# Kernel tuning notes

Hardware: AMD Instinct MI355X
Metric: run time of the kernel (lower is better)

Reference implementation:

```python
import jax, jax.numpy as jnp
import numpy as np

N_NODES = 100000
N_EDGES = 1600000
D_IN = 128
D_OUT = 128


def setup_inputs() -> dict:
    key = jax.random.key(0)
    k1, k2, k3 = jax.random.split(key, 3)
    x = jax.random.normal(k1, (N_NODES, D_IN), dtype=jnp.float32)
    edge_indices = jax.random.randint(k2, (2, N_EDGES), 0, N_NODES, dtype=jnp.int64)
    # nn.Linear(input_dim, output_dim, bias=False): weight shape [out, in]
    W = jax.random.normal(k3, (D_OUT, D_IN), dtype=jnp.float32) * (1.0 / np.sqrt(D_IN))
    return {"x": x, "edge_indices": edge_indices, "W": W}


def reference(x, edge_indices, W):
    N = x.shape[0]
    # add self loops (i, i) for every node, as in create_norm_adj_mat
    self_loops = jnp.arange(N, dtype=edge_indices.dtype)
    row = jnp.concatenate([edge_indices[0], self_loops])  # [E+N]
    col = jnp.concatenate([edge_indices[1], self_loops])  # [E+N]
    # degree from row indices (torch.bincount(edge_indices[0]))
    deg = jax.ops.segment_sum(jnp.ones_like(row, dtype=x.dtype), row, num_segments=N)
    deg_rsqrt = jax.lax.rsqrt(deg)  # every node has a self loop -> deg >= 1
    vals = deg_rsqrt[row] * deg_rsqrt[col]  # [E+N] edge weights
    # dense linear projection first (linear(x)), then sparse aggregation
    h = x @ W.T  # [N, D_OUT]
    # (norm_adj_mat @ h)[i] = sum over edges with row==i of vals * h[col]
    agg = jax.ops.segment_sum(vals[:, None] * h[col], row, num_segments=N)  # [N, D_OUT]
    return jax.nn.relu(agg)
```

## Files before the change

### kernel.cpp

```cpp
#include <hip/hip_runtime.h>
#include <hip/hip_bf16.h>

#define D 128
#define SH 8
#define BROWS 256
#define NBK_MAX 512
#define CH 8192

typedef __bf16   bf16x8 __attribute__((ext_vector_type(8)));
typedef float    f32x4  __attribute__((ext_vector_type(4)));
typedef _Float16 f16x2  __attribute__((ext_vector_type(2)));
typedef _Float16 f16x4  __attribute__((ext_vector_type(4)));

__global__ __launch_bounds__(256) void k_zero(int* __restrict__ p, int n) {
    for (int i = blockIdx.x * blockDim.x + threadIdx.x; i < n; i += gridDim.x * blockDim.x)
        p[i] = 0;
}

__global__ __launch_bounds__(256) void k_bucket_count(const int* __restrict__ rows,
                                                      int* __restrict__ bcnt, int E, int NBK) {
    __shared__ int h[NBK_MAX];
    for (int i = threadIdx.x; i < NBK; i += 256) h[i] = 0;
    __syncthreads();
    for (int e = blockIdx.x * blockDim.x + threadIdx.x; e < E; e += gridDim.x * blockDim.x)
        atomicAdd(&h[rows[e] >> SH], 1);
    __syncthreads();
    for (int i = threadIdx.x; i < NBK; i += 256) {
        int v = h[i];
        if (v) atomicAdd(&bcnt[i], v);
    }
}

__global__ __launch_bounds__(512) void k_scan_buckets(const int* __restrict__ bcnt,
                                                      int* __restrict__ boff,
                                                      int* __restrict__ bcur, int NBK, int E) {
    __shared__ int sd[512];
    int t = threadIdx.x;
    int own = (t < NBK) ? bcnt[t] : 0;
    sd[t] = own;
    __syncthreads();
    for (int off = 1; off < 512; off <<= 1) {
        int add = (t >= off) ? sd[t - off] : 0;
        __syncthreads();
        sd[t] += add;
        __syncthreads();
    }
    if (t < NBK) {
        int ex = sd[t] - own;
        boff[t] = ex;
        bcur[t] = ex;
    }
    if (t == 0) boff[NBK] = E;
}

__global__ __launch_bounds__(256) void k_pairs(const int* __restrict__ rows,
                                               const int* __restrict__ cols,
                                               int* __restrict__ bcur,
                                               unsigned* __restrict__ pairs, int E, int NBK) {
    __shared__ int h[NBK_MAX];
    int e0 = blockIdx.x * CH;
    if (e0 >= E) return;
    int e1 = min(E, e0 + CH);
    for (int i = threadIdx.x; i < NBK; i += 256) h[i] = 0;
    __syncthreads();
    for (int e = e0 + threadIdx.x; e < e1; e += 256)
        atomicAdd(&h[rows[e] >> SH], 1);
    __syncthreads();
    for (int b = threadIdx.x; b < NBK; b += 256) {
        int v = h[b];
        h[b] = v ? atomicAdd(&bcur[b], v) : 0;
    }
    __syncthreads();
    for (int e = e0 + threadIdx.x; e < e1; e += 256) {
        int r = rows[e];
        int b = r >> SH;
        int p = atomicAdd(&h[b], 1);
        pairs[p] = ((unsigned)(r & (BROWS - 1)) << 24) | (unsigned)cols[e];
    }
}

__global__ __launch_bounds__(256) void k_bucket_hist(const unsigned* __restrict__ pairs,
                                                     const int* __restrict__ boff,
                                                     int* __restrict__ cnt, int N) {
    __shared__ int h[BROWS];
    int b = blockIdx.x;
    int lim = min(N - (b << SH), BROWS);
    h[threadIdx.x] = 0;
    __syncthreads();
    int p0 = boff[b], p1 = boff[b + 1];
    for (int p = p0 + threadIdx.x; p < p1; p += 256)
        atomicAdd(&h[pairs[p] >> 24], 1);
    __syncthreads();
    if (threadIdx.x < lim) cnt[(b << SH) + threadIdx.x] = h[threadIdx.x];
}

__global__ __launch_bounds__(256) void k_chunk_sum(const int* __restrict__ cnt,
                                                   int* __restrict__ bsum, int N) {
    __shared__ int sd[256];
    int base = blockIdx.x * 1024;
    int t = threadIdx.x;
    int s = 0;
#pragma unroll
    for (int k = 0; k < 4; ++k) {
        int i = base + t * 4 + k;
        if (i < N) s += cnt[i];
    }
    sd[t] = s;
    __syncthreads();
    for (int off = 128; off > 0; off >>= 1) {
        if (t < off) sd[t] += sd[t + off];
        __syncthreads();
    }
    if (t == 0) bsum[blockIdx.x] = sd[0];
}

__global__ __launch_bounds__(1024) void k_scan_tops(const int* __restrict__ bsum,
                                                    int* __restrict__ boff2, int nb,
                                                    int* __restrict__ row_start, int N, int E) {
    __shared__ int sd[1024];
    int t = threadIdx.x;
    int own = (t < nb) ? bsum[t] : 0;
    sd[t] = own;
    __syncthreads();
    for (int off = 1; off < 1024; off <<= 1) {
        int add = (t >= off) ? sd[t - off] : 0;
        __syncthreads();
        sd[t] += add;
        __syncthreads();
    }
    if (t < nb) boff2[t] = sd[t] - own;
    if (t == 0) row_start[N] = E;
}

__global__ __launch_bounds__(256) void k_scan_chunk(const int* __restrict__ cnt,
                                                    const int* __restrict__ boff2,
                                                    int* __restrict__ row_start,
                                                    float* __restrict__ dr, int N) {
    __shared__ int tsum[256];
    int base = blockIdx.x * 1024;
    int t = threadIdx.x;
    int v[4];
    int s = 0;
#pragma unroll
    for (int k = 0; k < 4; ++k) {
        int i = base + t * 4 + k;
        v[k] = (i < N) ? cnt[i] : 0;
        s += v[k];
    }
    tsum[t] = s;
    __syncthreads();
    for (int off = 1; off < 256; off <<= 1) {
        int add = (t >= off) ? tsum[t - off] : 0;
        __syncthreads();
        tsum[t] += add;
        __syncthreads();
    }
    int run = boff2[blockIdx.x] + tsum[t] - s;
#pragma unroll
    for (int k = 0; k < 4; ++k) {
        int i = base + t * 4 + k;
        if (i < N) {
            row_start[i] = run;
            dr[i] = rsqrtf((float)(v[k] + 1));
            run += v[k];
        }
    }
}

__global__ __launch_bounds__(256) void k_place(const unsigned* __restrict__ pairs,
                                               const int* __restrict__ boff,
                                               const int* __restrict__ row_start,
                                               int* __restrict__ csr_col, int N) {
    __shared__ int cur[BROWS];
    int b = blockIdx.x;
    int lim = min(N - (b << SH), BROWS);
    if (threadIdx.x < lim) cur[threadIdx.x] = row_start[(b << SH) + threadIdx.x];
    __syncthreads();
    int p0 = boff[b], p1 = boff[b + 1];
    for (int p = p0 + threadIdx.x; p < p1; p += 256) {
        unsigned v = pairs[p];
        int rl = v >> 24;
        int c  = v & 0xFFFFFF;
        int q = atomicAdd(&cur[rl], 1);
        csr_col[q] = c;
    }
}

__global__ __launch_bounds__(256) void k_half(const float4* __restrict__ x4,
                                              f16x4* __restrict__ xh4, int n4) {
    for (int i = blockIdx.x * blockDim.x + threadIdx.x; i < n4; i += gridDim.x * blockDim.x) {
        float4 v = x4[i];
        xh4[i] = (f16x4){(_Float16)v.x, (_Float16)v.y, (_Float16)v.z, (_Float16)v.w};
    }
}

__global__ __launch_bounds__(256) void k_gather_h(const int* __restrict__ row_start,
                                                  const int* __restrict__ csr_col,
                                                  const _Float16* __restrict__ xh,
                                                  const float* __restrict__ dr,
                                                  float* __restrict__ out, int N) {
    int lane = threadIdx.x & 63;
    int gw = (blockIdx.x * blockDim.x + threadIdx.x) >> 6;
    int nw = (gridDim.x * blockDim.x) >> 6;
    for (int r = gw; r < N; r += nw) {
        float drr = dr[r];
        int beg = row_start[r], end = row_start[r + 1];
        const f16x2 xs = *(const f16x2*)&xh[(size_t)r * D + lane * 2];
        float s = drr * drr;
        float a0 = s * (float)xs[0], a1 = s * (float)xs[1];
        for (int cb = beg; cb < end; cb += 64) {
            int m = end - cb;
            if (m > 64) m = 64;
            int   cidx = (lane < m) ? csr_col[cb + lane] : 0;
            float cdr  = (lane < m) ? dr[cidx] : 0.f;
            int j = 0;
            for (; j + 8 <= m; j += 8) {
#pragma unroll
                for (int u = 0; u < 8; u += 4) {
                    int c0 = __shfl(cidx, j + u);
                    int c1 = __shfl(cidx, j + u + 1);
                    int c2 = __shfl(cidx, j + u + 2);
                    int c3 = __shfl(cidx, j + u + 3);
                    float v0 = drr * __shfl(cdr, j + u);
                    float v1 = drr * __shfl(cdr, j + u + 1);
                    float v2 = drr * __shfl(cdr, j + u + 2);
                    float v3 = drr * __shfl(cdr, j + u + 3);
                    const f16x2 p0 = *(const f16x2*)&xh[(size_t)c0 * D + lane * 2];
                    const f16x2 p1 = *(const f16x2*)&xh[(size_t)c1 * D + lane * 2];
                    const f16x2 p2 = *(const f16x2*)&xh[(size_t)c2 * D + lane * 2];
                    const f16x2 p3 = *(const f16x2*)&xh[(size_t)c3 * D + lane * 2];
                    a0 = fmaf(v0, (float)p0[0], a0); a1 = fmaf(v0, (float)p0[1], a1);
                    a0 = fmaf(v1, (float)p1[0], a0); a1 = fmaf(v1, (float)p1[1], a1);
                    a0 = fmaf(v2, (float)p2[0], a0); a1 = fmaf(v2, (float)p2[1], a1);
                    a0 = fmaf(v3, (float)p3[0], a0); a1 = fmaf(v3, (float)p3[1], a1);
                }
            }
            for (; j < m; ++j) {
                int   c = __shfl(cidx, j);
                float v = drr * __shfl(cdr, j);
                const f16x2 p = *(const f16x2*)&xh[(size_t)c * D + lane * 2];
                a0 = fmaf(v, (float)p[0], a0);
                a1 = fmaf(v, (float)p[1], a1);
            }
        }
        float2 o;
        o.x = a0;
        o.y = a1;
        *(float2*)&out[(size_t)r * D + lane * 2] = o;
    }
}

__global__ __launch_bounds__(256) void k_gather(const int* __restrict__ row_start,
                                                const int* __restrict__ csr_col,
                                                const float* __restrict__ x,
                                                const float* __restrict__ dr,
                                                float* __restrict__ out, int N) {
    int lane = threadIdx.x & 63;
    int gw = (blockIdx.x * blockDim.x + threadIdx.x) >> 6;
    int nw = (gridDim.x * blockDim.x) >> 6;
    for (int r = gw; r < N; r += nw) {
        float drr = dr[r];
        int beg = row_start[r], end = row_start[r + 1];
        const float2 xs = *(const float2*)&x[(size_t)r * D + lane * 2];
        float s = drr * drr;
        float a0 = s * xs.x, a1 = s * xs.y;
        for (int cb = beg; cb < end; cb += 64) {
            int m = end - cb;
            if (m > 64) m = 64;
            int   cidx = (lane < m) ? csr_col[cb + lane] : 0;
            float cdr  = (lane < m) ? dr[cidx] : 0.f;
            int j = 0;
            for (; j + 4 <= m; j += 4) {
                int c0 = __shfl(cidx, j);
                int c1 = __shfl(cidx, j + 1);
                int c2 = __shfl(cidx, j + 2);
                int c3 = __shfl(cidx, j + 3);
                float v0 = drr * __shfl(cdr, j);
                float v1 = drr * __shfl(cdr, j + 1);
                float v2 = drr * __shfl(cdr, j + 2);
                float v3 = drr * __shfl(cdr, j + 3);
                const float2 p0 = *(const float2*)&x[(size_t)c0 * D + lane * 2];
                const float2 p1 = *(const float2*)&x[(size_t)c1 * D + lane * 2];
                const float2 p2 = *(const float2*)&x[(size_t)c2 * D + lane * 2];
                const float2 p3 = *(const float2*)&x[(size_t)c3 * D + lane * 2];
                a0 = fmaf(v0, p0.x, a0); a1 = fmaf(v0, p0.y, a1);
                a0 = fmaf(v1, p1.x, a0); a1 = fmaf(v1, p1.y, a1);
                a0 = fmaf(v2, p2.x, a0); a1 = fmaf(v2, p2.y, a1);
                a0 = fmaf(v3, p3.x, a0); a1 = fmaf(v3, p3.y, a1);
            }
            for (; j < m; ++j) {
                int   c = __shfl(cidx, j);
                float v = drr * __shfl(cdr, j);
                const float2 p = *(const float2*)&x[(size_t)c * D + lane * 2];
                a0 = fmaf(v, p.x, a0);
                a1 = fmaf(v, p.y, a1);
            }
        }
        float2 o;
        o.x = a0;
        o.y = a1;
        *(float2*)&out[(size_t)r * D + lane * 2] = o;
    }
}

#define CT 8
#define KS 4

__global__ __launch_bounds__(256) void k_project_mfma(const float* __restrict__ W,
                                                      float* __restrict__ out, int N) {
    __shared__ bf16x8 Bhi[CT * KS * 64];
    __shared__ bf16x8 Blo[CT * KS * 64];

    for (int f = threadIdx.x; f < CT * KS * 64; f += 256) {
        int l  = f & 63;
        int ks = (f >> 6) & 3;
        int ct = f >> 8;
        int o  = ct * 16 + (l & 15);
        int k0 = ks * 32 + ((l >> 4) * 8);
        const float* src = &W[o * D + k0];
        bf16x8 hi, lo;
#pragma unroll
        for (int i = 0; i < 8; ++i) {
            float v  = src[i];
            __bf16 h = (__bf16)v;
            float  r = v - (float)h;
            hi[i] = h;
            lo[i] = (__bf16)r;
        }
        Bhi[f] = hi;
        Blo[f] = lo;
    }
    __syncthreads();

    int lane = threadIdx.x & 63;
    int wib  = threadIdx.x >> 6;
    int gw   = blockIdx.x * 4 + wib;
    int nw   = gridDim.x * 4;
    int nt   = N >> 4;

    int arow  = lane & 15;
    int kbase = (lane >> 4) * 8;

    for (int t = gw; t < nt; t += nw) {
        int row = t * 16 + arow;
        const float* arp = &out[(size_t)row * D + kbase];

        bf16x8 Ahi[KS], Alo[KS];
#pragma unroll
        for (int ks = 0; ks < KS; ++ks) {
            float4 v0 = *(const float4*)&arp[ks * 32];
            float4 v1 = *(const float4*)&arp[ks * 32 + 4];
            float va[8] = {v0.x, v0.y, v0.z, v0.w, v1.x, v1.y, v1.z, v1.w};
            bf16x8 hi, lo;
#pragma unroll
            for (int i = 0; i < 8; ++i) {
                float v  = va[i];
                __bf16 h = (__bf16)v;
                float  r = v - (float)h;
                hi[i] = h;
                lo[i] = (__bf16)r;
            }
            Ahi[ks] = hi;
            Alo[ks] = lo;
        }

        f32x4 acc[CT];
#pragma unroll
        for (int ct = 0; ct < CT; ++ct) acc[ct] = (f32x4){0.f, 0.f, 0.f, 0.f};

#pragma unroll
        for (int ks = 0; ks < KS; ++ks) {
#pragma unroll
            for (int ct = 0; ct < CT; ++ct) {
                bf16x8 bh = Bhi[(ct * KS + ks) * 64 + lane];
                bf16x8 bl = Blo[(ct * KS + ks) * 64 + lane];
                acc[ct] = __builtin_amdgcn_mfma_f32_16x16x32_bf16(Ahi[ks], bh, acc[ct], 0, 0, 0);
                acc[ct] = __builtin_amdgcn_mfma_f32_16x16x32_bf16(Alo[ks], bh, acc[ct], 0, 0, 0);
                acc[ct] = __builtin_amdgcn_mfma_f32_16x16x32_bf16(Ahi[ks], bl, acc[ct], 0, 0, 0);
            }
        }

        int orow = t * 16 + (lane >> 4) * 4;
        int ocol = lane & 15;
#pragma unroll
        for (int ct = 0; ct < CT; ++ct) {
#pragma unroll
            for (int reg = 0; reg < 4; ++reg) {
                out[(size_t)(orow + reg) * D + ct * 16 + ocol] = fmaxf(acc[ct][reg], 0.f);
            }
        }
    }
}

__global__ __launch_bounds__(256) void k_init_deg(int* __restrict__ deg, int n) {
    for (int i = blockIdx.x * blockDim.x + threadIdx.x; i < n; i += gridDim.x * blockDim.x)
        deg[i] = 1;
}
__global__ __launch_bounds__(256) void k_count_atomic(const int* __restrict__ rows,
                                                      int* __restrict__ cnt, int E) {
    for (int e = blockIdx.x * blockDim.x + threadIdx.x; e < E; e += gridDim.x * blockDim.x)
        atomicAdd(&cnt[rows[e]], 1);
}
__global__ __launch_bounds__(256) void k_rsqrt(float* __restrict__ buf, int n) {
    const int* di = (const int*)buf;
    for (int i = blockIdx.x * blockDim.x + threadIdx.x; i < n; i += gridDim.x * blockDim.x) {
        int v = di[i];
        buf[i] = rsqrtf((float)v);
    }
}
__global__ __launch_bounds__(256) void k_init_out(const float4* __restrict__ x4,
                                                  const float* __restrict__ dr,
                                                  float4* __restrict__ out4, int n4) {
    for (int i = blockIdx.x * blockDim.x + threadIdx.x; i < n4; i += gridDim.x * blockDim.x) {
        float d = dr[i >> 5];
        float s = d * d;
        float4 v = x4[i];
        out4[i] = make_float4(v.x * s, v.y * s, v.z * s, v.w * s);
    }
}
__global__ __launch_bounds__(256) void k_edges(const int* __restrict__ rows,
                                               const int* __restrict__ cols,
                                               const float* __restrict__ x,
                                               const float* __restrict__ dr,
                                               float* __restrict__ out, int E) {
    int lane = threadIdx.x & 63;
    int wib  = threadIdx.x >> 6;
    int gw   = blockIdx.x * 4 + wib;
    int nw   = gridDim.x * 4;
    for (int e = gw; e < E; e += nw) {
        int r = rows[e];
        int c = cols[e];
        float val = dr[r] * dr[c];
        const float2 xv = *(const float2*)&x[(size_t)c * D + lane * 2];
        float* po = &out[(size_t)r * D + lane * 2];
        unsafeAtomicAdd(po,     val * xv.x);
        unsafeAtomicAdd(po + 1, val * xv.y);
    }
}

extern "C" void kernel_launch(void* const* d_in, const int* in_sizes, int n_in,
                              void* d_out, int out_size, void* d_ws, size_t ws_size,
                              hipStream_t stream) {
    const float* x   = (const float*)d_in[0];
    const int*   idx = (const int*)d_in[1];
    const float* W   = (const float*)d_in[2];
    float*       out = (float*)d_out;

    int N = in_sizes[0] / D;
    int E = in_sizes[1] / 2;
    const int* rows = idx;
    const int* cols = idx + E;

    int NBK = (N + BROWS - 1) >> SH;
    int nb  = (N + 1023) / 1024;

    size_t off = 0;
    size_t o_pairs = off;  off += (size_t)E;
    size_t o_csr   = off;  off += (size_t)E;
    size_t o_cnt   = off;  off += (size_t)N;
    size_t o_rs    = off;  off += (size_t)N + 1;
    size_t o_dr    = off;  off += (size_t)N;
    size_t o_bsum  = off;  off += (size_t)nb;
    size_t o_boff2 = off;  off += (size_t)nb;
    size_t o_bcnt  = off;  off += (size_t)NBK;
    size_t o_boff  = off;  off += (size_t)NBK + 1;
    size_t o_bcur  = off;  off += (size_t)NBK;
    off = (off + 3) & ~(size_t)3;
    size_t o_xh    = off;  off += ((size_t)N * D) / 2;
    size_t need_full = off * 4;
    size_t need_base = o_xh * 4;

    int* wsw = (int*)d_ws;

    bool shape_ok = (NBK <= NBK_MAX) && (nb <= 1024) && ((N & 15) == 0) && (N < (1 << 24));

    if (shape_ok && ws_size >= need_base) {
        unsigned* pairs     = (unsigned*)(wsw + o_pairs);
        int*      csr_col   = wsw + o_csr;
        int*      cnt       = wsw + o_cnt;
        int*      row_start = wsw + o_rs;
        float*    dr        = (float*)(wsw + o_dr);
        int*      bsum      = wsw + o_bsum;
        int*      boff2     = wsw + o_boff2;
        int*      bcnt      = wsw + o_bcnt;
        int*      boff      = wsw + o_boff;
        int*      bcur      = wsw + o_bcur;
        _Float16* xh        = (_Float16*)(wsw + o_xh);

        k_zero<<<(NBK + 255) / 256, 256, 0, stream>>>(bcnt, NBK);
        k_bucket_count<<<512, 256, 0, stream>>>(rows, bcnt, E, NBK);
        k_scan_buckets<<<1, 512, 0, stream>>>(bcnt, boff, bcur, NBK, E);
        k_pairs<<<(E + CH - 1) / CH, 256, 0, stream>>>(rows, cols, bcur, pairs, E, NBK);
        k_bucket_hist<<<NBK, 256, 0, stream>>>(pairs, boff, cnt, N);
        k_chunk_sum<<<nb, 256, 0, stream>>>(cnt, bsum, N);
        k_scan_tops<<<1, 1024, 0, stream>>>(bsum, boff2, nb, row_start, N, E);
        k_scan_chunk<<<nb, 256, 0, stream>>>(cnt, boff2, row_start, dr, N);
        k_place<<<NBK, 256, 0, stream>>>(pairs, boff, row_start, csr_col, N);

        if (ws_size >= need_full) {
            k_half<<<2048, 256, 0, stream>>>((const float4*)x, (f16x4*)xh, N * (D / 4));
            k_gather_h<<<4096, 256, 0, stream>>>(row_start, csr_col, xh, dr, out, N);
        } else {
            k_gather<<<4096, 256, 0, stream>>>(row_start, csr_col, x, dr, out, N);
        }
        int nt = N >> 4;
        k_project_mfma<<<(nt + 3) / 4, 256, 0, stream>>>(W, out, N);
    } else {
        int*   deg = (int*)d_ws;
        float* dr  = (float*)d_ws;
        k_init_deg<<<(N + 255) / 256, 256, 0, stream>>>(deg, N);
        k_count_atomic<<<2048, 256, 0, stream>>>(rows, deg, E);
        k_rsqrt<<<(N + 255) / 256, 256, 0, stream>>>(dr, N);
        int n4 = N * (D / 4);
        k_init_out<<<4096, 256, 0, stream>>>((const float4*)x, dr, (float4*)out, n4);
        k_edges<<<4096, 256, 0, stream>>>(rows, cols, x, dr, out, E);
        int nt = N >> 4;
        k_project_mfma<<<(nt + 3) / 4, 256, 0, stream>>>(W, out, N);
    }
}
```

Before: 230.3 us.

## Fuse gather aggregation with MFMA projection and prescale fp16 features by degree

```diff
diff --git a/kernel.cpp b/kernel.cpp
--- a/kernel.cpp
+++ b/kernel.cpp
@@ -6,11 +6,13 @@
 #define BROWS 256
 #define NBK_MAX 512
 #define CH 8192
+#define CT 8
+#define KS 4
 
 typedef __bf16   bf16x8 __attribute__((ext_vector_type(8)));
 typedef float    f32x4  __attribute__((ext_vector_type(4)));
-typedef _Float16 f16x2  __attribute__((ext_vector_type(2)));
 typedef _Float16 f16x4  __attribute__((ext_vector_type(4)));
+typedef _Float16 f16x8  __attribute__((ext_vector_type(8)));
 
 __global__ __launch_bounds__(256) void k_zero(int* __restrict__ p, int n) {
     for (int i = blockIdx.x * blockDim.x + threadIdx.x; i < n; i += gridDim.x * blockDim.x)
@@ -186,67 +188,166 @@
     }
 }
 
-__global__ __launch_bounds__(256) void k_half(const float4* __restrict__ x4,
-                                              f16x4* __restrict__ xh4, int n4) {
+__global__ __launch_bounds__(256) void k_half_s(const float4* __restrict__ x4,
+                                                const float* __restrict__ dr,
+                                                f16x4* __restrict__ xh4, int n4) {
     for (int i = blockIdx.x * blockDim.x + threadIdx.x; i < n4; i += gridDim.x * blockDim.x) {
+        float d = dr[i >> 5];
         float4 v = x4[i];
-        xh4[i] = (f16x4){(_Float16)v.x, (_Float16)v.y, (_Float16)v.z, (_Float16)v.w};
-    }
-}
-
-__global__ __launch_bounds__(256) void k_gather_h(const int* __restrict__ row_start,
-                                                  const int* __restrict__ csr_col,
-                                                  const _Float16* __restrict__ xh,
-                                                  const float* __restrict__ dr,
-                                                  float* __restrict__ out, int N) {
+        xh4[i] = (f16x4){(_Float16)(v.x * d), (_Float16)(v.y * d),
+                         (_Float16)(v.z * d), (_Float16)(v.w * d)};
+    }
+}
+
+__global__ __launch_bounds__(256) void k_prepW(const float* __restrict__ W,
+                                               bf16x8* __restrict__ Whi,
+                                               bf16x8* __restrict__ Wlo) {
+    for (int f = blockIdx.x * blockDim.x + threadIdx.x; f < CT * KS * 64;
+         f += gridDim.x * blockDim.x) {
+        int l  = f & 63;
+        int ks = (f >> 6) & 3;
+        int ct = f >> 8;
+        int o  = ct * 16 + (l & 15);
+        int k0 = ks * 32 + ((l >> 4) * 8);
+        const float* src = &W[o * D + k0];
+        bf16x8 hi, lo;
+#pragma unroll
+        for (int i = 0; i < 8; ++i) {
+            float v  = src[i];
+            __bf16 h = (__bf16)v;
+            hi[i] = h;
+            lo[i] = (__bf16)(v - (float)h);
+        }
+        Whi[f] = hi;
+        Wlo[f] = lo;
+    }
+}
+
+__global__ __launch_bounds__(256) void k_gp(const int* __restrict__ row_start,
+                                            const int* __restrict__ csr_col,
+                                            const _Float16* __restrict__ xh,
+                                            const float* __restrict__ dr,
+                                            const bf16x8* __restrict__ Whi,
+                                            const bf16x8* __restrict__ Wlo,
+                                            float* __restrict__ out, int NT) {
+    __shared__ float lds[4][16][132];
     int lane = threadIdx.x & 63;
+    int wib  = threadIdx.x >> 6;
+    float (*patch)[132] = lds[wib];
+
     int gw = (blockIdx.x * blockDim.x + threadIdx.x) >> 6;
     int nw = (gridDim.x * blockDim.x) >> 6;
-    for (int r = gw; r < N; r += nw) {
-        float drr = dr[r];
-        int beg = row_start[r], end = row_start[r + 1];
-        const f16x2 xs = *(const f16x2*)&xh[(size_t)r * D + lane * 2];
-        float s = drr * drr;
-        float a0 = s * (float)xs[0], a1 = s * (float)xs[1];
-        for (int cb = beg; cb < end; cb += 64) {
-            int m = end - cb;
-            if (m > 64) m = 64;
-            int   cidx = (lane < m) ? csr_col[cb + lane] : 0;
-            float cdr  = (lane < m) ? dr[cidx] : 0.f;
-            int j = 0;
-            for (; j + 8 <= m; j += 8) {
-#pragma unroll
-                for (int u = 0; u < 8; u += 4) {
-                    int c0 = __shfl(cidx, j + u);
-                    int c1 = __shfl(cidx, j + u + 1);
-                    int c2 = __shfl(cidx, j + u + 2);
-                    int c3 = __shfl(cidx, j + u + 3);
-                    float v0 = drr * __shfl(cdr, j + u);
-                    float v1 = drr * __shfl(cdr, j + u + 1);
-                    float v2 = drr * __shfl(cdr, j + u + 2);
-                    float v3 = drr * __shfl(cdr, j + u + 3);
-                    const f16x2 p0 = *(const f16x2*)&xh[(size_t)c0 * D + lane * 2];
-                    const f16x2 p1 = *(const f16x2*)&xh[(size_t)c1 * D + lane * 2];
-                    const f16x2 p2 = *(const f16x2*)&xh[(size_t)c2 * D + lane * 2];
-                    const f16x2 p3 = *(const f16x2*)&xh[(size_t)c3 * D + lane * 2];
-                    a0 = fmaf(v0, (float)p0[0], a0); a1 = fmaf(v0, (float)p0[1], a1);
-                    a0 = fmaf(v1, (float)p1[0], a0); a1 = fmaf(v1, (float)p1[1], a1);
-                    a0 = fmaf(v2, (float)p2[0], a0); a1 = fmaf(v2, (float)p2[1], a1);
-                    a0 = fmaf(v3, (float)p3[0], a0); a1 = fmaf(v3, (float)p3[1], a1);
+
+    int eslot = lane >> 4;
+    int dbase = (lane & 15) * 8;
+
+    for (int t = gw; t < NT; t += nw) {
+        int r0 = t * 16;
+        int   rs16 = (lane < 17) ? row_start[r0 + lane] : 0;
+        float dr16 = (lane < 16) ? dr[r0 + lane] : 0.f;
+
+        for (int rr = 0; rr < 16; ++rr) {
+            int r   = r0 + rr;
+            int beg = __shfl(rs16, rr);
+            int end = __shfl(rs16, rr + 1);
+            float drr = __shfl(dr16, rr);
+
+            float acc[8];
+            {
+                f16x8 xs = *(const f16x8*)&xh[(size_t)r * D + dbase];
+                float w = (eslot == 0) ? 1.0f : 0.0f;
+#pragma unroll
+                for (int i = 0; i < 8; ++i) acc[i] = w * (float)xs[i];
+            }
+
+            for (int cb = beg; cb < end; cb += 64) {
+                int m = end - cb;
+                if (m > 64) m = 64;
+                int cidx = (lane < m) ? csr_col[cb + lane] : 0;
+                int g = 0;
+                for (; g + 16 <= m; g += 16) {
+                    int c0 = __shfl(cidx, g + eslot);
+                    int c1 = __shfl(cidx, g + 4 + eslot);
+                    int c2 = __shfl(cidx, g + 8 + eslot);
+                    int c3 = __shfl(cidx, g + 12 + eslot);
+                    f16x8 p0 = *(const f16x8*)&xh[(size_t)c0 * D + dbase];
+                    f16x8 p1 = *(const f16x8*)&xh[(size_t)c1 * D + dbase];
+                    f16x8 p2 = *(const f16x8*)&xh[(size_t)c2 * D + dbase];
+                    f16x8 p3 = *(const f16x8*)&xh[(size_t)c3 * D + dbase];
+#pragma unroll
+                    for (int i = 0; i < 8; ++i) {
+                        acc[i] += (float)p0[i] + (float)p1[i];
+                        acc[i] += (float)p2[i] + (float)p3[i];
+                    }
                 }
-            }
-            for (; j < m; ++j) {
-                int   c = __shfl(cidx, j);
-                float v = drr * __shfl(cdr, j);
-                const f16x2 p = *(const f16x2*)&xh[(size_t)c * D + lane * 2];
-                a0 = fmaf(v, (float)p[0], a0);
-                a1 = fmaf(v, (float)p[1], a1);
-            }
-        }
-        float2 o;
-        o.x = a0;
-        o.y = a1;
-        *(float2*)&out[(size_t)r * D + lane * 2] = o;
+                for (; g < m; g += 4) {
+                    int src = g + eslot;
+                    bool valid = (src < m);
+                    int c = __shfl(cidx, valid ? src : 0);
+                    int cc = valid ? c : r;
+                    f16x8 pv = *(const f16x8*)&xh[(size_t)cc * D + dbase];
+                    float w = valid ? 1.0f : 0.0f;
+#pragma unroll
+                    for (int i = 0; i < 8; ++i) acc[i] = fmaf(w, (float)pv[i], acc[i]);
+                }
+            }
+
+#pragma unroll
+            for (int i = 0; i < 8; ++i) {
+                acc[i] += __shfl_xor(acc[i], 16);
+                acc[i] += __shfl_xor(acc[i], 32);
+                acc[i] *= drr;
+            }
+            if (lane < 16) {
+                *(float4*)&patch[rr][dbase]     = make_float4(acc[0], acc[1], acc[2], acc[3]);
+                *(float4*)&patch[rr][dbase + 4] = make_float4(acc[4], acc[5], acc[6], acc[7]);
+            }
+        }
+
+        int arow  = lane & 15;
+        int kbase = (lane >> 4) * 8;
+        bf16x8 Ahi[KS], Alo[KS];
+#pragma unroll
+        for (int ks = 0; ks < KS; ++ks) {
+            int k0 = ks * 32 + kbase;
+            float4 v0 = *(const float4*)&patch[arow][k0];
+            float4 v1 = *(const float4*)&patch[arow][k0 + 4];
+            float va[8] = {v0.x, v0.y, v0.z, v0.w, v1.x, v1.y, v1.z, v1.w};
+            bf16x8 hi, lo;
+#pragma unroll
+            for (int i = 0; i < 8; ++i) {
+                __bf16 h = (__bf16)va[i];
+                hi[i] = h;
+                lo[i] = (__bf16)(va[i] - (float)h);
+            }
+            Ahi[ks] = hi;
+            Alo[ks] = lo;
+        }
+
+        f32x4 acc4[CT];
+#pragma unroll
+        for (int ct = 0; ct < CT; ++ct) acc4[ct] = (f32x4){0.f, 0.f, 0.f, 0.f};
+#pragma unroll
+        for (int ks = 0; ks < KS; ++ks) {
+#pragma unroll
+            for (int ct = 0; ct < CT; ++ct) {
+                bf16x8 bh = Whi[(ct * KS + ks) * 64 + lane];
+                bf16x8 bl = Wlo[(ct * KS + ks) * 64 + lane];
+                acc4[ct] = __builtin_amdgcn_mfma_f32_16x16x32_bf16(Ahi[ks], bh, acc4[ct], 0, 0, 0);
+                acc4[ct] = __builtin_amdgcn_mfma_f32_16x16x32_bf16(Alo[ks], bh, acc4[ct], 0, 0, 0);
+                acc4[ct] = __builtin_amdgcn_mfma_f32_16x16x32_bf16(Ahi[ks], bl, acc4[ct], 0, 0, 0);
+            }
+        }
+
+        int orow = r0 + (lane >> 4) * 4;
+        int ocol = lane & 15;
+#pragma unroll
+        for (int ct = 0; ct < CT; ++ct) {
+#pragma unroll
+            for (int reg = 0; reg < 4; ++reg) {
+                out[(size_t)(orow + reg) * D + ct * 16 + ocol] = fmaxf(acc4[ct][reg], 0.f);
+            }
+        }
     }
 }
 
@@ -303,14 +404,10 @@
     }
 }
 
-#define CT 8
-#define KS 4
-
 __global__ __launch_bounds__(256) void k_project_mfma(const float* __restrict__ W,
                                                       float* __restrict__ out, int N) {
     __shared__ bf16x8 Bhi[CT * KS * 64];
     __shared__ bf16x8 Blo[CT * KS * 64];
-
     for (int f = threadIdx.x; f < CT * KS * 64; f += 256) {
         int l  = f & 63;
         int ks = (f >> 6) & 3;
@@ -323,9 +420,8 @@
         for (int i = 0; i < 8; ++i) {
             float v  = src[i];
             __bf16 h = (__bf16)v;
-            float  r = v - (float)h;
             hi[i] = h;
-            lo[i] = (__bf16)r;
+            lo[i] = (__bf16)(v - (float)h);
         }
         Bhi[f] = hi;
         Blo[f] = lo;
@@ -337,14 +433,12 @@
     int gw   = blockIdx.x * 4 + wib;
     int nw   = gridDim.x * 4;
     int nt   = N >> 4;
-
     int arow  = lane & 15;
     int kbase = (lane >> 4) * 8;
 
     for (int t = gw; t < nt; t += nw) {
         int row = t * 16 + arow;
         const float* arp = &out[(size_t)row * D + kbase];
-
         bf16x8 Ahi[KS], Alo[KS];
 #pragma unroll
         for (int ks = 0; ks < KS; ++ks) {
@@ -354,20 +448,16 @@
             bf16x8 hi, lo;
 #pragma unroll
             for (int i = 0; i < 8; ++i) {
-                float v  = va[i];
-                __bf16 h = (__bf16)v;
-                float  r = v - (float)h;
+                __bf16 h = (__bf16)va[i];
                 hi[i] = h;
-                lo[i] = (__bf16)r;
+                lo[i] = (__bf16)(va[i] - (float)h);
             }
             Ahi[ks] = hi;
             Alo[ks] = lo;
         }
-
         f32x4 acc[CT];
 #pragma unroll
         for (int ct = 0; ct < CT; ++ct) acc[ct] = (f32x4){0.f, 0.f, 0.f, 0.f};
-
 #pragma unroll
         for (int ks = 0; ks < KS; ++ks) {
 #pragma unroll
@@ -379,7 +469,6 @@
                 acc[ct] = __builtin_amdgcn_mfma_f32_16x16x32_bf16(Ahi[ks], bl, acc[ct], 0, 0, 0);
             }
         }
-
         int orow = t * 16 + (lane >> 4) * 4;
         int ocol = lane & 15;
 #pragma unroll
@@ -466,15 +555,16 @@
     size_t o_boff  = off;  off += (size_t)NBK + 1;
     size_t o_bcur  = off;  off += (size_t)NBK;
     off = (off + 3) & ~(size_t)3;
+    size_t need_mid = off * 4;
+    size_t o_whi   = off;  off += (size_t)(CT * KS * 64) * 4;
+    size_t o_wlo   = off;  off += (size_t)(CT * KS * 64) * 4;
     size_t o_xh    = off;  off += ((size_t)N * D) / 2;
     size_t need_full = off * 4;
-    size_t need_base = o_xh * 4;
 
     int* wsw = (int*)d_ws;
-
     bool shape_ok = (NBK <= NBK_MAX) && (nb <= 1024) && ((N & 15) == 0) && (N < (1 << 24));
 
-    if (shape_ok && ws_size >= need_base) {
+    if (shape_ok && ws_size >= need_mid) {
         unsigned* pairs     = (unsigned*)(wsw + o_pairs);
         int*      csr_col   = wsw + o_csr;
         int*      cnt       = wsw + o_cnt;
@@ -485,7 +575,6 @@
         int*      bcnt      = wsw + o_bcnt;
         int*      boff      = wsw + o_boff;
         int*      bcur      = wsw + o_bcur;
-        _Float16* xh        = (_Float16*)(wsw + o_xh);
 
         k_zero<<<(NBK + 255) / 256, 256, 0, stream>>>(bcnt, NBK);
         k_bucket_count<<<512, 256, 0, stream>>>(rows, bcnt, E, NBK);
@@ -498,13 +587,18 @@
         k_place<<<NBK, 256, 0, stream>>>(pairs, boff, row_start, csr_col, N);
 
         if (ws_size >= need_full) {
-            k_half<<<2048, 256, 0, stream>>>((const float4*)x, (f16x4*)xh, N * (D / 4));
-            k_gather_h<<<4096, 256, 0, stream>>>(row_start, csr_col, xh, dr, out, N);
+            bf16x8*   Whi = (bf16x8*)(wsw + o_whi);
+            bf16x8*   Wlo = (bf16x8*)(wsw + o_wlo);
+            _Float16* xh  = (_Float16*)(wsw + o_xh);
+            k_prepW<<<8, 256, 0, stream>>>(W, Whi, Wlo);
+            k_half_s<<<2048, 256, 0, stream>>>((const float4*)x, dr, (f16x4*)xh, N * (D / 4));
+            int NT = N >> 4;
+            k_gp<<<(NT + 3) / 4, 256, 0, stream>>>(row_start, csr_col, xh, dr, Whi, Wlo, out, NT);
         } else {
             k_gather<<<4096, 256, 0, stream>>>(row_start, csr_col, x, dr, out, N);
-        }
-        int nt = N >> 4;
-        k_project_mfma<<<(nt + 3) / 4, 256, 0, stream>>>(W, out, N);
+            int nt = N >> 4;
+            k_project_mfma<<<(nt + 3) / 4, 256, 0, stream>>>(W, out, N);
+        }
     } else {
         int*   deg = (int*)d_ws;
         float* dr  = (float*)d_ws;
```

Result: slower. 344.5 us (+49.5%).

## Fuse CSR row-scan into bucket pass and prescale features by degree rsqrt

Applied to the files above, without the earlier changes.

```diff
diff --git a/kernel.cpp b/kernel.cpp
--- a/kernel.cpp
+++ b/kernel.cpp
@@ -6,6 +6,8 @@
 #define BROWS 256
 #define NBK_MAX 512
 #define CH 8192
+#define CT 8
+#define KS 4
 
 typedef __bf16   bf16x8 __attribute__((ext_vector_type(8)));
 typedef float    f32x4  __attribute__((ext_vector_type(4)));
@@ -33,7 +35,9 @@
 
 __global__ __launch_bounds__(512) void k_scan_buckets(const int* __restrict__ bcnt,
                                                       int* __restrict__ boff,
-                                                      int* __restrict__ bcur, int NBK, int E) {
+                                                      int* __restrict__ bcur,
+                                                      int* __restrict__ row_start,
+                                                      int NBK, int N, int E) {
     __shared__ int sd[512];
     int t = threadIdx.x;
     int own = (t < NBK) ? bcnt[t] : 0;
@@ -50,7 +54,10 @@
         boff[t] = ex;
         bcur[t] = ex;
     }
-    if (t == 0) boff[NBK] = E;
+    if (t == 0) {
+        boff[NBK] = E;
+        row_start[N] = E;
+    }
 }
 
 __global__ __launch_bounds__(256) void k_pairs(const int* __restrict__ rows,
@@ -79,122 +86,59 @@
     }
 }
 
-__global__ __launch_bounds__(256) void k_bucket_hist(const unsigned* __restrict__ pairs,
-                                                     const int* __restrict__ boff,
-                                                     int* __restrict__ cnt, int N) {
+__global__ __launch_bounds__(256) void k_bucket_finish(const unsigned* __restrict__ pairs,
+                                                       const int* __restrict__ boff,
+                                                       int* __restrict__ row_start,
+                                                       float* __restrict__ dr,
+                                                       int* __restrict__ csr_col, int N) {
     __shared__ int h[BROWS];
-    int b = blockIdx.x;
-    int lim = min(N - (b << SH), BROWS);
-    h[threadIdx.x] = 0;
-    __syncthreads();
-    int p0 = boff[b], p1 = boff[b + 1];
-    for (int p = p0 + threadIdx.x; p < p1; p += 256)
-        atomicAdd(&h[pairs[p] >> 24], 1);
-    __syncthreads();
-    if (threadIdx.x < lim) cnt[(b << SH) + threadIdx.x] = h[threadIdx.x];
-}
-
-__global__ __launch_bounds__(256) void k_chunk_sum(const int* __restrict__ cnt,
-                                                   int* __restrict__ bsum, int N) {
-    __shared__ int sd[256];
-    int base = blockIdx.x * 1024;
-    int t = threadIdx.x;
-    int s = 0;
-#pragma unroll
-    for (int k = 0; k < 4; ++k) {
-        int i = base + t * 4 + k;
-        if (i < N) s += cnt[i];
-    }
-    sd[t] = s;
-    __syncthreads();
-    for (int off = 128; off > 0; off >>= 1) {
-        if (t < off) sd[t] += sd[t + off];
-        __syncthreads();
-    }
-    if (t == 0) bsum[blockIdx.x] = sd[0];
-}
-
-__global__ __launch_bounds__(1024) void k_scan_tops(const int* __restrict__ bsum,
-                                                    int* __restrict__ boff2, int nb,
-                                                    int* __restrict__ row_start, int N, int E) {
-    __shared__ int sd[1024];
-    int t = threadIdx.x;
-    int own = (t < nb) ? bsum[t] : 0;
-    sd[t] = own;
-    __syncthreads();
-    for (int off = 1; off < 1024; off <<= 1) {
-        int add = (t >= off) ? sd[t - off] : 0;
-        __syncthreads();
-        sd[t] += add;
-        __syncthreads();
-    }
-    if (t < nb) boff2[t] = sd[t] - own;
-    if (t == 0) row_start[N] = E;
-}
-
-__global__ __launch_bounds__(256) void k_scan_chunk(const int* __restrict__ cnt,
-                                                    const int* __restrict__ boff2,
-                                                    int* __restrict__ row_start,
-                                                    float* __restrict__ dr, int N) {
-    __shared__ int tsum[256];
-    int base = blockIdx.x * 1024;
-    int t = threadIdx.x;
-    int v[4];
-    int s = 0;
-#pragma unroll
-    for (int k = 0; k < 4; ++k) {
-        int i = base + t * 4 + k;
-        v[k] = (i < N) ? cnt[i] : 0;
-        s += v[k];
-    }
-    tsum[t] = s;
-    __syncthreads();
-    for (int off = 1; off < 256; off <<= 1) {
-        int add = (t >= off) ? tsum[t - off] : 0;
-        __syncthreads();
-        tsum[t] += add;
-        __syncthreads();
-    }
-    int run = boff2[blockIdx.x] + tsum[t] - s;
-#pragma unroll
-    for (int k = 0; k < 4; ++k) {
-        int i = base + t * 4 + k;
-        if (i < N) {
-            row_start[i] = run;
-            dr[i] = rsqrtf((float)(v[k] + 1));
-            run += v[k];
-        }
-    }
-}
-
-__global__ __launch_bounds__(256) void k_place(const unsigned* __restrict__ pairs,
-                                               const int* __restrict__ boff,
-                                               const int* __restrict__ row_start,
-                                               int* __restrict__ csr_col, int N) {
     __shared__ int cur[BROWS];
     int b = blockIdx.x;
+    int t = threadIdx.x;
     int lim = min(N - (b << SH), BROWS);
-    if (threadIdx.x < lim) cur[threadIdx.x] = row_start[(b << SH) + threadIdx.x];
+    h[t] = 0;
     __syncthreads();
     int p0 = boff[b], p1 = boff[b + 1];
-    for (int p = p0 + threadIdx.x; p < p1; p += 256) {
+    for (int p = p0 + t; p < p1; p += 256)
+        atomicAdd(&h[pairs[p] >> 24], 1);
+    __syncthreads();
+    int own = h[t];
+    cur[t] = own;
+    __syncthreads();
+    for (int off = 1; off < 256; off <<= 1) {
+        int add = (t >= off) ? cur[t - off] : 0;
+        __syncthreads();
+        cur[t] += add;
+        __syncthreads();
+    }
+    int rs = p0 + cur[t] - own;
+    if (t < lim) {
+        row_start[(b << SH) + t] = rs;
+        dr[(b << SH) + t] = rsqrtf((float)(own + 1));
+    }
+    __syncthreads();
+    cur[t] = rs;
+    __syncthreads();
+    for (int p = p0 + t; p < p1; p += 256) {
         unsigned v = pairs[p];
         int rl = v >> 24;
-        int c  = v & 0xFFFFFF;
         int q = atomicAdd(&cur[rl], 1);
-        csr_col[q] = c;
-    }
-}
-
-__global__ __launch_bounds__(256) void k_half(const float4* __restrict__ x4,
-                                              f16x4* __restrict__ xh4, int n4) {
+        csr_col[q] = (int)(v & 0xFFFFFF);
+    }
+}
+
+__global__ __launch_bounds__(256) void k_half_s(const float4* __restrict__ x4,
+                                                const float* __restrict__ dr,
+                                                f16x4* __restrict__ xh4, int n4) {
     for (int i = blockIdx.x * blockDim.x + threadIdx.x; i < n4; i += gridDim.x * blockDim.x) {
+        float d = dr[i >> 5];
         float4 v = x4[i];
-        xh4[i] = (f16x4){(_Float16)v.x, (_Float16)v.y, (_Float16)v.z, (_Float16)v.w};
-    }
-}
-
-__global__ __launch_bounds__(256) void k_gather_h(const int* __restrict__ row_start,
+        xh4[i] = (f16x4){(_Float16)(v.x * d), (_Float16)(v.y * d),
+                         (_Float16)(v.z * d), (_Float16)(v.w * d)};
+    }
+}
+
+__global__ __launch_bounds__(256) void k_gather_s(const int* __restrict__ row_start,
                                                   const int* __restrict__ csr_col,
                                                   const _Float16* __restrict__ xh,
                                                   const float* __restrict__ dr,
@@ -206,47 +150,122 @@
         float drr = dr[r];
         int beg = row_start[r], end = row_start[r + 1];
         const f16x2 xs = *(const f16x2*)&xh[(size_t)r * D + lane * 2];
-        float s = drr * drr;
-        float a0 = s * (float)xs[0], a1 = s * (float)xs[1];
+        float a0 = (float)xs[0], a1 = (float)xs[1];
         for (int cb = beg; cb < end; cb += 64) {
             int m = end - cb;
             if (m > 64) m = 64;
-            int   cidx = (lane < m) ? csr_col[cb + lane] : 0;
-            float cdr  = (lane < m) ? dr[cidx] : 0.f;
+            int cidx = (lane < m) ? csr_col[cb + lane] : 0;
             int j = 0;
             for (; j + 8 <= m; j += 8) {
-#pragma unroll
-                for (int u = 0; u < 8; u += 4) {
-                    int c0 = __shfl(cidx, j + u);
-                    int c1 = __shfl(cidx, j + u + 1);
-                    int c2 = __shfl(cidx, j + u + 2);
-                    int c3 = __shfl(cidx, j + u + 3);
-                    float v0 = drr * __shfl(cdr, j + u);
-                    float v1 = drr * __shfl(cdr, j + u + 1);
-                    float v2 = drr * __shfl(cdr, j + u + 2);
-                    float v3 = drr * __shfl(cdr, j + u + 3);
-                    const f16x2 p0 = *(const f16x2*)&xh[(size_t)c0 * D + lane * 2];
-                    const f16x2 p1 = *(const f16x2*)&xh[(size_t)c1 * D + lane * 2];
-                    const f16x2 p2 = *(const f16x2*)&xh[(size_t)c2 * D + lane * 2];
-                    const f16x2 p3 = *(const f16x2*)&xh[(size_t)c3 * D + lane * 2];
-                    a0 = fmaf(v0, (float)p0[0], a0); a1 = fmaf(v0, (float)p0[1], a1);
-                    a0 = fmaf(v1, (float)p1[0], a0); a1 = fmaf(v1, (float)p1[1], a1);
-                    a0 = fmaf(v2, (float)p2[0], a0); a1 = fmaf(v2, (float)p2[1], a1);
-                    a0 = fmaf(v3, (float)p3[0], a0); a1 = fmaf(v3, (float)p3[1], a1);
-                }
+                int c0 = __shfl(cidx, j);
+                int c1 = __shfl(cidx, j + 1);
+                int c2 = __shfl(cidx, j + 2);
+                int c3 = __shfl(cidx, j + 3);
+                int c4 = __shfl(cidx, j + 4);
+                int c5 = __shfl(cidx, j + 5);
+                int c6 = __shfl(cidx, j + 6);
+                int c7 = __shfl(cidx, j + 7);
+                f16x2 p0 = *(const f16x2*)&xh[(size_t)c0 * D + lane * 2];
+                f16x2 p1 = *(const f16x2*)&xh[(size_t)c1 * D + lane * 2];
+                f16x2 p2 = *(const f16x2*)&xh[(size_t)c2 * D + lane * 2];
+                f16x2 p3 = *(const f16x2*)&xh[(size_t)c3 * D + lane * 2];
+                f16x2 p4 = *(const f16x2*)&xh[(size_t)c4 * D + lane * 2];
+                f16x2 p5 = *(const f16x2*)&xh[(size_t)c5 * D + lane * 2];
+                f16x2 p6 = *(const f16x2*)&xh[(size_t)c6 * D + lane * 2];
+                f16x2 p7 = *(const f16x2*)&xh[(size_t)c7 * D + lane * 2];
+                a0 += (float)p0[0] + (float)p1[0] + (float)p2[0] + (float)p3[0]
+                    + (float)p4[0] + (float)p5[0] + (float)p6[0] + (float)p7[0];
+                a1 += (float)p0[1] + (float)p1[1] + (float)p2[1] + (float)p3[1]
+                    + (float)p4[1] + (float)p5[1] + (float)p6[1] + (float)p7[1];
             }
             for (; j < m; ++j) {
-                int   c = __shfl(cidx, j);
-                float v = drr * __shfl(cdr, j);
-                const f16x2 p = *(const f16x2*)&xh[(size_t)c * D + lane * 2];
-                a0 = fmaf(v, (float)p[0], a0);
-                a1 = fmaf(v, (float)p[1], a1);
+                int c = __shfl(cidx, j);
+                f16x2 p = *(const f16x2*)&xh[(size_t)c * D + lane * 2];
+                a0 += (float)p[0];
+                a1 += (float)p[1];
             }
         }
         float2 o;
-        o.x = a0;
-        o.y = a1;
+        o.x = drr * a0;
+        o.y = drr * a1;
         *(float2*)&out[(size_t)r * D + lane * 2] = o;
+    }
+}
+
+__global__ __launch_bounds__(256) void k_project_mfma(const float* __restrict__ W,
+                                                      float* __restrict__ out, int N) {
+    __shared__ bf16x8 Bhi[CT * KS * 64];
+    __shared__ bf16x8 Blo[CT * KS * 64];
+    for (int f = threadIdx.x; f < CT * KS * 64; f += 256) {
+        int l  = f & 63;
+        int ks = (f >> 6) & 3;
+        int ct = f >> 8;
+        int o  = ct * 16 + (l & 15);
+        int k0 = ks * 32 + ((l >> 4) * 8);
+        const float* src = &W[o * D + k0];
+        bf16x8 hi, lo;
+#pragma unroll
+        for (int i = 0; i < 8; ++i) {
+            float v  = src[i];
+            __bf16 h = (__bf16)v;
+            hi[i] = h;
+            lo[i] = (__bf16)(v - (float)h);
+        }
+        Bhi[f] = hi;
+        Blo[f] = lo;
+    }
+    __syncthreads();
+
+    int lane = threadIdx.x & 63;
+    int wib  = threadIdx.x >> 6;
+    int gw   = blockIdx.x * 4 + wib;
+    int nw   = gridDim.x * 4;
+    int nt   = N >> 4;
+    int arow  = lane & 15;
+    int kbase = (lane >> 4) * 8;
+
+    for (int t = gw; t < nt; t += nw) {
+        int row = t * 16 + arow;
+        const float* arp = &out[(size_t)row * D + kbase];
+        bf16x8 Ahi[KS], Alo[KS];
+#pragma unroll
+        for (int ks = 0; ks < KS; ++ks) {
+            float4 v0 = *(const float4*)&arp[ks * 32];
+            float4 v1 = *(const float4*)&arp[ks * 32 + 4];
+            float va[8] = {v0.x, v0.y, v0.z, v0.w, v1.x, v1.y, v1.z, v1.w};
+            bf16x8 hi, lo;
+#pragma unroll
+            for (int i = 0; i < 8; ++i) {
+                __bf16 h = (__bf16)va[i];
+                hi[i] = h;
+                lo[i] = (__bf16)(va[i] - (float)h);
+            }
+            Ahi[ks] = hi;
+            Alo[ks] = lo;
+        }
+        f32x4 acc[CT];
+#pragma unroll
+        for (int ct = 0; ct < CT; ++ct) acc[ct] = (f32x4){0.f, 0.f, 0.f, 0.f};
+#pragma unroll
+        for (int ks = 0; ks < KS; ++ks) {
+#pragma unroll
+            for (int ct = 0; ct < CT; ++ct) {
+                bf16x8 bh = Bhi[(ct * KS + ks) * 64 + lane];
+                bf16x8 bl = Blo[(ct * KS + ks) * 64 + lane];
+                acc[ct] = __builtin_amdgcn_mfma_f32_16x16x32_bf16(Ahi[ks], bh, acc[ct], 0, 0, 0);
+                acc[ct] = __builtin_amdgcn_mfma_f32_16x16x32_bf16(Alo[ks], bh, acc[ct], 0, 0, 0);
+                acc[ct] = __builtin_amdgcn_mfma_f32_16x16x32_bf16(Ahi[ks], bl, acc[ct], 0, 0, 0);
+            }
+        }
+        int orow = t * 16 + (lane >> 4) * 4;
+        int ocol = lane & 15;
+#pragma unroll
+        for (int ct = 0; ct < CT; ++ct) {
+#pragma unroll
+            for (int reg = 0; reg < 4; ++reg) {
+                out[(size_t)(orow + reg) * D + ct * 16 + ocol] = fmaxf(acc[ct][reg], 0.f);
+            }
+        }
     }
 }
 
@@ -303,95 +322,6 @@
     }
 }
 
-#define CT 8
-#define KS 4
-
-__global__ __launch_bounds__(256) void k_project_mfma(const float* __restrict__ W,
-                                                      float* __restrict__ out, int N) {
-    __shared__ bf16x8 Bhi[CT * KS * 64];
-    __shared__ bf16x8 Blo[CT * KS * 64];
-
-    for (int f = threadIdx.x; f < CT * KS * 64; f += 256) {
-        int l  = f & 63;
-        int ks = (f >> 6) & 3;
-        int ct = f >> 8;
-        int o  = ct * 16 + (l & 15);
-        int k0 = ks * 32 + ((l >> 4) * 8);
-        const float* src = &W[o * D + k0];
-        bf16x8 hi, lo;
-#pragma unroll
-        for (int i = 0; i < 8; ++i) {
-            float v  = src[i];
-            __bf16 h = (__bf16)v;
-            float  r = v - (float)h;
-            hi[i] = h;
-            lo[i] = (__bf16)r;
-        }
-        Bhi[f] = hi;
-        Blo[f] = lo;
-    }
-    __syncthreads();
-
-    int lane = threadIdx.x & 63;
-    int wib  = threadIdx.x >> 6;
-    int gw   = blockIdx.x * 4 + wib;
-    int nw   = gridDim.x * 4;
-    int nt   = N >> 4;
-
-    int arow  = lane & 15;
-    int kbase = (lane >> 4) * 8;
-
-    for (int t = gw; t < nt; t += nw) {
-        int row = t * 16 + arow;
-        const float* arp = &out[(size_t)row * D + kbase];
-
-        bf16x8 Ahi[KS], Alo[KS];
-#pragma unroll
-        for (int ks = 0; ks < KS; ++ks) {
-            float4 v0 = *(const float4*)&arp[ks * 32];
-            float4 v1 = *(const float4*)&arp[ks * 32 + 4];
-            float va[8] = {v0.x, v0.y, v0.z, v0.w, v1.x, v1.y, v1.z, v1.w};
-            bf16x8 hi, lo;
-#pragma unroll
-            for (int i = 0; i < 8; ++i) {
-                float v  = va[i];
-                __bf16 h = (__bf16)v;
-                float  r = v - (float)h;
-                hi[i] = h;
-                lo[i] = (__bf16)r;
-            }
-            Ahi[ks] = hi;
-            Alo[ks] = lo;
-        }
-
-        f32x4 acc[CT];
-#pragma unroll
-        for (int ct = 0; ct < CT; ++ct) acc[ct] = (f32x4){0.f, 0.f, 0.f, 0.f};
-
-#pragma unroll
-        for (int ks = 0; ks < KS; ++ks) {
-#pragma unroll
-            for (int ct = 0; ct < CT; ++ct) {
-                bf16x8 bh = Bhi[(ct * KS + ks) * 64 + lane];
-                bf16x8 bl = Blo[(ct * KS + ks) * 64 + lane];
-                acc[ct] = __builtin_amdgcn_mfma_f32_16x16x32_bf16(Ahi[ks], bh, acc[ct], 0, 0, 0);
-                acc[ct] = __builtin_amdgcn_mfma_f32_16x16x32_bf16(Alo[ks], bh, acc[ct], 0, 0, 0);
-                acc[ct] = __builtin_amdgcn_mfma_f32_16x16x32_bf16(Ahi[ks], bl, acc[ct], 0, 0, 0);
-            }
-        }
-
-        int orow = t * 16 + (lane >> 4) * 4;
-        int ocol = lane & 15;
-#pragma unroll
-        for (int ct = 0; ct < CT; ++ct) {
-#pragma unroll
-            for (int reg = 0; reg < 4; ++reg) {
-                out[(size_t)(orow + reg) * D + ct * 16 + ocol] = fmaxf(acc[ct][reg], 0.f);
-            }
-        }
-    }
-}
-
 __global__ __launch_bounds__(256) void k_init_deg(int* __restrict__ deg, int n) {
     for (int i = blockIdx.x * blockDim.x + threadIdx.x; i < n; i += gridDim.x * blockDim.x)
         deg[i] = 1;
@@ -452,54 +382,42 @@
     const int* cols = idx + E;
 
     int NBK = (N + BROWS - 1) >> SH;
-    int nb  = (N + 1023) / 1024;
 
     size_t off = 0;
     size_t o_pairs = off;  off += (size_t)E;
     size_t o_csr   = off;  off += (size_t)E;
-    size_t o_cnt   = off;  off += (size_t)N;
     size_t o_rs    = off;  off += (size_t)N + 1;
     size_t o_dr    = off;  off += (size_t)N;
-    size_t o_bsum  = off;  off += (size_t)nb;
-    size_t o_boff2 = off;  off += (size_t)nb;
     size_t o_bcnt  = off;  off += (size_t)NBK;
     size_t o_boff  = off;  off += (size_t)NBK + 1;
     size_t o_bcur  = off;  off += (size_t)NBK;
     off = (off + 3) & ~(size_t)3;
+    size_t need_mid = off * 4;
     size_t o_xh    = off;  off += ((size_t)N * D) / 2;
     size_t need_full = off * 4;
-    size_t need_base = o_xh * 4;
 
     int* wsw = (int*)d_ws;
-
-    bool shape_ok = (NBK <= NBK_MAX) && (nb <= 1024) && ((N & 15) == 0) && (N < (1 << 24));
-
-    if (shape_ok && ws_size >= need_base) {
+    bool shape_ok = (NBK <= NBK_MAX) && ((N & 15) == 0) && (N < (1 << 24));
+
+    if (shape_ok && ws_size >= need_mid) {
         unsigned* pairs     = (unsigned*)(wsw + o_pairs);
         int*      csr_col   = wsw + o_csr;
-        int*      cnt       = wsw + o_cnt;
         int*      row_start = wsw + o_rs;
         float*    dr        = (float*)(wsw + o_dr);
-        int*      bsum      = wsw + o_bsum;
-        int*      boff2     = wsw + o_boff2;
         int*      bcnt      = wsw + o_bcnt;
         int*      boff      = wsw + o_boff;
         int*      bcur      = wsw + o_bcur;
-        _Float16* xh        = (_Float16*)(wsw + o_xh);
 
         k_zero<<<(NBK + 255) / 256, 256, 0, stream>>>(bcnt, NBK);
         k_bucket_count<<<512, 256, 0, stream>>>(rows, bcnt, E, NBK);
-        k_scan_buckets<<<1, 512, 0, stream>>>(bcnt, boff, bcur, NBK, E);
+        k_scan_buckets<<<1, 512, 0, stream>>>(bcnt, boff, bcur, row_start, NBK, N, E);
         k_pairs<<<(E + CH - 1) / CH, 256, 0, stream>>>(rows, cols, bcur, pairs, E, NBK);
-        k_bucket_hist<<<NBK, 256, 0, stream>>>(pairs, boff, cnt, N);
-        k_chunk_sum<<<nb, 256, 0, stream>>>(cnt, bsum, N);
-        k_scan_tops<<<1, 1024, 0, stream>>>(bsum, boff2, nb, row_start, N, E);
-        k_scan_chunk<<<nb, 256, 0, stream>>>(cnt, boff2, row_start, dr, N);
-        k_place<<<NBK, 256, 0, stream>>>(pairs, boff, row_start, csr_col, N);
+        k_bucket_finish<<<NBK, 256, 0, stream>>>(pairs, boff, row_start, dr, csr_col, N);
 
         if (ws_size >= need_full) {
-            k_half<<<2048, 256, 0, stream>>>((const float4*)x, (f16x4*)xh, N * (D / 4));
-            k_gather_h<<<4096, 256, 0, stream>>>(row_start, csr_col, xh, dr, out, N);
+            _Float16* xh = (_Float16*)(wsw + o_xh);
+            k_half_s<<<2048, 256, 0, stream>>>((const float4*)x, dr, (f16x4*)xh, N * (D / 4));
+            k_gather_s<<<4096, 256, 0, stream>>>(row_start, csr_col, xh, dr, out, N);
         } else {
             k_gather<<<4096, 256, 0, stream>>>(row_start, csr_col, x, dr, out, N);
         }
```

New measurement: 219.2 us. -4.8%, faster.
